# Kernel optimization log

Hardware: AMD Instinct MI355X
Metric: run time of the kernel (lower is better)

The kernel has to match this reference:

```python
import jax, jax.numpy as jnp
import numpy as np

WS = 7    # window_size
SS = 3    # shift_size
NH = 12   # num_heads


def _rel_index(ws):
    # doublestepseq(2*Ww-1, Wh, 1, Ww): seq1[:,None]+seq2[None,:] -> (1, N)
    seq1 = np.arange(ws) * (2 * ws - 1)
    coords = (seq1[:, None] + np.arange(ws)[None, :]).reshape(1, -1)  # (1, N)
    rel = coords + coords.T          # (N, N)
    return np.ascontiguousarray(rel[:, ::-1])  # flip along axis 1


def _attn_mask(Hp, Wp, ws, ss):
    img = np.zeros((Hp, Wp), np.int32)
    cnt = 0
    for h in (slice(0, -ws), slice(-ws, -ss), slice(-ss, None)):
        for w in (slice(0, -ws), slice(-ws, -ss), slice(-ss, None)):
            img[h, w] = cnt
            cnt += 1
    mw = img.reshape(Hp // ws, ws, Wp // ws, ws).transpose(0, 2, 1, 3).reshape(-1, ws * ws)
    diff = mw[:, None, :] - mw[:, :, None]  # unsqueeze(1) - unsqueeze(2)
    return np.where(diff != 0, -100.0, 0.0).astype(np.float32)  # (nW, N, N)


def setup_inputs() -> dict:
    key = jax.random.key(0)
    ks = jax.random.split(key, 4)
    B, H, W, C = 8, 112, 112, 384
    x = jax.random.normal(ks[0], (B, H * W, C), jnp.float32)
    qkv_w = jax.random.normal(ks[1], (C, 3 * C), jnp.float32) * 0.02
    qkv_b = jnp.zeros((3 * C,), jnp.float32)
    proj_w = jax.random.normal(ks[2], (C, C), jnp.float32) * 0.02
    proj_b = jnp.zeros((C,), jnp.float32)
    rel_pos_table = jax.random.normal(ks[3], ((2 * WS - 1) ** 2, NH), jnp.float32) * 0.02
    return {"x": x, "qkv_w": qkv_w, "qkv_b": qkv_b, "proj_w": proj_w,
            "proj_b": proj_b, "rel_pos_table": rel_pos_table, "H": H, "W": W}


def reference(x, qkv_w, qkv_b, proj_w, proj_b, rel_pos_table, H, W):
    B, L, C = x.shape
    hd = C // NH
    scale = hd ** -0.5
    N = WS * WS
    q = x.reshape(B, H, W, C)
    pad_r = (WS - W % WS) % WS
    pad_b = (WS - H % WS) % WS
    q = jnp.pad(q, ((0, 0), (0, pad_b), (0, pad_r), (0, 0)))
    Hp, Wp = H + pad_b, W + pad_r
    # cyclic shift
    sq = jnp.roll(q, (-SS, -SS), axis=(1, 2))
    nWh, nWw = Hp // WS, Wp // WS
    nW = nWh * nWw
    # window partition -> (B*nW, N, C)
    win = sq.reshape(B, nWh, WS, nWw, WS, C).transpose(0, 1, 3, 2, 4, 5).reshape(-1, N, C)
    Bw = win.shape[0]
    qkv = (win @ qkv_w + qkv_b).reshape(Bw, N, 3, NH, hd).transpose(2, 0, 3, 1, 4)
    qh, kh, vh = qkv[0], qkv[1], qkv[2]          # (Bw, NH, N, hd)
    attn = jnp.einsum('whnd,whmd->whnm', qh * scale, kh)  # (Bw, NH, N, N)
    # relative position bias
    ridx = _rel_index(WS)
    bias = rel_pos_table[ridx.reshape(-1)].reshape(N, N, NH).transpose(2, 0, 1)
    attn = attn + bias[None]
    # shifted-window mask
    mask = jnp.asarray(_attn_mask(Hp, Wp, WS, SS))  # (nW, N, N)
    attn = attn.reshape(B, nW, NH, N, N) + mask[None, :, None]
    attn = jax.nn.softmax(attn.reshape(Bw, NH, N, N), axis=-1)
    out = jnp.einsum('whnm,whmd->whnd', attn, vh).transpose(0, 2, 1, 3).reshape(Bw, N, C)
    out = out @ proj_w + proj_b
    # window reverse + reverse shift
    sx = out.reshape(B, nWh, nWw, WS, WS, C).transpose(0, 1, 3, 2, 4, 5).reshape(B, Hp, Wp, C)
    xr = jnp.roll(sx, (SS, SS), axis=(1, 2))[:, :H, :W, :]
    return xr.reshape(B, H * W, C)
```

## Files before the change

kernel.cpp:

```cpp
#include <hip/hip_runtime.h>


typedef __bf16 bf16;
typedef __bf16 bf16x8 __attribute__((ext_vector_type(8)));
typedef float  f32x4  __attribute__((ext_vector_type(4)));

#define MFMA16(a, b, c) __builtin_amdgcn_mfma_f32_16x16x32_bf16((a), (b), (c), 0, 0, 0)

static __device__ __forceinline__ bf16x8 cvt8(const float4 lo, const float4 hi) {
    bf16x8 r;
    r[0] = (bf16)lo.x; r[1] = (bf16)lo.y; r[2] = (bf16)lo.z; r[3] = (bf16)lo.w;
    r[4] = (bf16)hi.x; r[5] = (bf16)hi.y; r[6] = (bf16)hi.z; r[7] = (bf16)hi.w;
    return r;
}

__global__ __launch_bounds__(256) void k0_prep(
    const float* __restrict__ qkv_w, const float* __restrict__ proj_w,
    const float* __restrict__ rpt,
    bf16* __restrict__ w1t, bf16* __restrict__ w2t, float* __restrict__ BT)
{
    unsigned tid = blockIdx.x * 256u + threadIdx.x;
    if (tid < 442368u) {
        unsigned n = tid / 384u, k = tid - n * 384u;
        float v = qkv_w[k * 1152u + n];
        if (n < 384u) v *= 0.17677669529663687f;
        w1t[tid] = (bf16)v;
    } else if (tid < 589824u) {
        unsigned i = tid - 442368u;
        unsigned n = i / 384u, k = i - n * 384u;
        w2t[i] = (bf16)proj_w[k * 384u + n];
    } else if (tid < 638976u) {
        unsigned i = tid - 589824u;
        unsigned h = i >> 12, r = i & 4095u, b = r >> 6, a = r & 63u;
        float v;
        if (b >= 49u) v = -1e9f;
        else if (a >= 49u) v = 0.0f;
        else {
            int ia = (int)(a / 7u), ja = (int)(a - 7u * (a / 7u));
            int ib = (int)(b / 7u), jb = (int)(b - 7u * (b / 7u));
            int ridx = 84 + 13 * (ia - ib) + (ja - jb);
            v = rpt[ridx * 12 + (int)h];
        }
        BT[i] = v;
    }
}

__global__ __launch_bounds__(256) void k0x_cvt(
    const float* __restrict__ X, bf16* __restrict__ Xb)
{
    size_t base = ((size_t)blockIdx.x * 256u + threadIdx.x) * 8u;
    float4 lo = *(const float4*)(X + base);
    float4 hi = *(const float4*)(X + base + 4);
    *(bf16x8*)(Xb + base) = cvt8(lo, hi);
}

__global__ __launch_bounds__(256, 3) void k1_qkv_b(
    const bf16* __restrict__ X, const bf16* __restrict__ W,
    const float* __restrict__ bias, bf16* __restrict__ Y)
{
    __shared__ __align__(16) bf16 Bs[24576];
    unsigned id = blockIdx.x;
    unsigned xcd = id & 7u, seq = id >> 3;
    unsigned mi = seq / 18u, nb = seq - mi * 18u;
    unsigned mblk = xcd + (mi << 3);
    unsigned tid = threadIdx.x;
    unsigned lane = tid & 63u, wv = tid >> 6;
    unsigned ln = lane & 15u, lq = lane >> 4;
    unsigned m0 = mblk * 256u, n0 = nb * 64u;

    for (unsigned c = tid; c < 3072u; c += 256u) {
        unsigned row = c / 48u, kc = c - row * 48u, k = kc * 8u;
        unsigned blk = (k >> 5) * 4u + (row >> 4);
        unsigned l = (row & 15u) | ((kc & 3u) << 4);
        *(int4*)&Bs[(blk * 64u + l) * 8u] = *(const int4*)(W + (size_t)(n0 + row) * 384u + k);
    }
    __syncthreads();

    f32x4 acc[4][4] = {};
    unsigned rbase = m0 + wv * 64u;
    const bf16* Ab = X + (size_t)(rbase + ln) * 384u + lq * 8u;

    bf16x8 af[3][4];
#pragma unroll
    for (unsigned i = 0; i < 4; ++i) af[0][i] = *(const bf16x8*)(Ab + i * 6144u);
#pragma unroll
    for (unsigned i = 0; i < 4; ++i) af[1][i] = *(const bf16x8*)(Ab + 32u + i * 6144u);

#pragma unroll
    for (unsigned kt = 0; kt < 12; ++kt) {
        if (kt < 10u) {
#pragma unroll
            for (unsigned i = 0; i < 4; ++i)
                af[(kt + 2u) % 3u][i] =
                    *(const bf16x8*)(Ab + (kt + 2u) * 32u + i * 6144u);
        }
        bf16x8 bfr[4];
#pragma unroll
        for (unsigned j = 0; j < 4; ++j)
            bfr[j] = *(const bf16x8*)&Bs[((kt * 4u + j) * 64u + lane) * 8u];
#pragma unroll
        for (unsigned i = 0; i < 4; ++i)
#pragma unroll
            for (unsigned j = 0; j < 4; ++j)
                acc[i][j] = MFMA16(af[kt % 3u][i], bfr[j], acc[i][j]);
    }

    float bv[4];
#pragma unroll
    for (unsigned j = 0; j < 4; ++j) {
        unsigned col = n0 + j * 16u + ln;
        bv[j] = bias[col];
        if (col < 384u) bv[j] *= 0.17677669529663687f;
    }

    __syncthreads();
#pragma unroll
    for (unsigned i = 0; i < 4; ++i)
#pragma unroll
        for (unsigned j = 0; j < 4; ++j)
#pragma unroll
            for (unsigned rg = 0; rg < 4; ++rg) {
                unsigned r = wv * 64u + i * 16u + lq * 4u + rg;
                Bs[r * 72u + j * 16u + ln] = (bf16)(acc[i][j][rg] + bv[j]);
            }
    __syncthreads();

#pragma unroll
    for (unsigned it = 0; it < 8; ++it) {
        unsigned idx = it * 256u + tid;
        unsigned row = idx >> 3, c8 = (idx & 7u) * 8u;
        *(bf16x8*)(Y + (size_t)(m0 + row) * 1152u + n0 + c8) =
            *(const bf16x8*)&Bs[row * 72u + c8];
    }
}

__global__ __launch_bounds__(256, 3) void k1_qkv(
    const float* __restrict__ X, const bf16* __restrict__ W,
    const float* __restrict__ bias, bf16* __restrict__ Y)
{
    __shared__ __align__(16) bf16 Bs[24576];
    unsigned id = blockIdx.x;
    unsigned xcd = id & 7u, seq = id >> 3;
    unsigned mi = seq / 18u, nb = seq - mi * 18u;
    unsigned mblk = xcd + (mi << 3);
    unsigned tid = threadIdx.x;
    unsigned lane = tid & 63u, wv = tid >> 6;
    unsigned ln = lane & 15u, lq = lane >> 4;
    unsigned m0 = mblk * 256u, n0 = nb * 64u;

    for (unsigned c = tid; c < 3072u; c += 256u) {
        unsigned row = c / 48u, kc = c - row * 48u, k = kc * 8u;
        unsigned blk = (k >> 5) * 4u + (row >> 4);
        unsigned l = (row & 15u) | ((kc & 3u) << 4);
        *(int4*)&Bs[(blk * 64u + l) * 8u] = *(const int4*)(W + (size_t)(n0 + row) * 384u + k);
    }
    __syncthreads();

    f32x4 acc[4][4] = {};
    unsigned rbase = m0 + wv * 64u;

#pragma unroll
    for (unsigned kt = 0; kt < 12; ++kt) {
        bf16x8 af[4], bfr[4];
#pragma unroll
        for (unsigned i = 0; i < 4; ++i) {
            const float* p = X + (size_t)(rbase + i * 16u + ln) * 384u + kt * 32u + lq * 8u;
            af[i] = cvt8(*(const float4*)p, *(const float4*)(p + 4));
        }
#pragma unroll
        for (unsigned j = 0; j < 4; ++j)
            bfr[j] = *(const bf16x8*)&Bs[((kt * 4u + j) * 64u + lane) * 8u];
#pragma unroll
        for (unsigned i = 0; i < 4; ++i)
#pragma unroll
            for (unsigned j = 0; j < 4; ++j)
                acc[i][j] = MFMA16(af[i], bfr[j], acc[i][j]);
    }

#pragma unroll
    for (unsigned j = 0; j < 4; ++j) {
        unsigned col = n0 + j * 16u + ln;
        float bv = bias[col];
        if (col < 384u) bv *= 0.17677669529663687f;
#pragma unroll
        for (unsigned i = 0; i < 4; ++i) {
            unsigned row = rbase + i * 16u + lq * 4u;
#pragma unroll
            for (unsigned rg = 0; rg < 4; ++rg)
                Y[(size_t)(row + rg) * 1152u + col] = (bf16)(acc[i][j][rg] + bv);
        }
    }
}

__global__ __launch_bounds__(64) void k2_attn(
    bf16* __restrict__ Y, const float* __restrict__ BT)
{
    __shared__ __align__(16) bf16 Pl[64 * 72];
    __shared__ __align__(16) bf16 Vt[32 * 72];
    unsigned h = blockIdx.x, bwin = blockIdx.y;
    unsigned bb = bwin >> 8, wi = bwin & 255u, wh = wi >> 4, ww = wi & 15u;
    unsigned lane = threadIdx.x, ln = lane & 15u, lq = lane >> 4;
    unsigned hw32 = h * 32u;

    auto pixrow = [&](unsigned t) -> unsigned {
        unsigned ti = t / 7u, tj = t - ti * 7u;
        unsigned gh = wh * 7u + ti + 3u; if (gh >= 112u) gh -= 112u;
        unsigned gw = ww * 7u + tj + 3u; if (gw >= 112u) gw -= 112u;
        return bb * 12544u + gh * 112u + gw;
    };

    {
        unsigned t = lane < 49u ? lane : 0u;
        const bf16* vs = Y + (size_t)pixrow(t) * 1152u + 768u + hw32;
        bf16x8 v0 = *(const bf16x8*)(vs);
        bf16x8 v1 = *(const bf16x8*)(vs + 8);
        bf16x8 v2 = *(const bf16x8*)(vs + 16);
        bf16x8 v3 = *(const bf16x8*)(vs + 24);
#pragma unroll
        for (int d = 0; d < 8; ++d) {
            Vt[(unsigned)(d     ) * 72u + lane] = v0[d];
            Vt[(unsigned)(d + 8 ) * 72u + lane] = v1[d];
            Vt[(unsigned)(d + 16) * 72u + lane] = v2[d];
            Vt[(unsigned)(d + 24) * 72u + lane] = v3[d];
        }
    }

    bf16x8 qf[4], kf[4];
#pragma unroll
    for (int i = 0; i < 4; ++i) {
        unsigned t = (unsigned)i * 16u + ln; t = t < 49u ? t : 0u;
        qf[i] = *(const bf16x8*)(Y + (size_t)pixrow(t) * 1152u + hw32 + lq * 8u);
    }
#pragma unroll
    for (int i = 0; i < 4; ++i) {
        unsigned t = (unsigned)i * 16u + ln; t = t < 49u ? t : 0u;
        kf[i] = *(const bf16x8*)(Y + (size_t)pixrow(t) * 1152u + 384u + hw32 + lq * 8u);
    }

    f32x4 s[4][4] = {};
#pragma unroll
    for (int i = 0; i < 4; ++i)
#pragma unroll
        for (int j = 0; j < 4; ++j)
            s[i][j] = MFMA16(qf[i], kf[j], s[i][j]);

    const float* bth = BT + h * 4096u;
#pragma unroll
    for (int i = 0; i < 4; ++i)
#pragma unroll
        for (int j = 0; j < 4; ++j) {
            f32x4 b = *(const f32x4*)(bth + ((unsigned)j * 16u + ln) * 64u +
                                      (unsigned)i * 16u + lq * 4u);
            s[i][j] += b;
        }

    if (wh == 15u || ww == 15u) {
        int ra[4][4], rb[4];
#pragma unroll
        for (int i = 0; i < 4; ++i)
#pragma unroll
            for (int rg = 0; rg < 4; ++rg) {
                unsigned a = (unsigned)i * 16u + lq * 4u + (unsigned)rg;
                unsigned ti = a / 7u, tj = a - ti * 7u;
                unsigned gh = wh * 7u + ti, gw = ww * 7u + tj;
                int rh = gh < 105u ? 0 : (gh < 109u ? 1 : 2);
                int rw = gw < 105u ? 0 : (gw < 109u ? 1 : 2);
                ra[i][rg] = rh * 3 + rw;
            }
#pragma unroll
        for (int j = 0; j < 4; ++j) {
            unsigned bc = (unsigned)j * 16u + ln;
            unsigned ti = bc / 7u, tj = bc - ti * 7u;
            unsigned gh = wh * 7u + ti, gw = ww * 7u + tj;
            int rh = gh < 105u ? 0 : (gh < 109u ? 1 : 2);
            int rw = gw < 105u ? 0 : (gw < 109u ? 1 : 2);
            rb[j] = rh * 3 + rw;
        }
#pragma unroll
        for (int i = 0; i < 4; ++i)
#pragma unroll
            for (int j = 0; j < 4; ++j)
#pragma unroll
                for (int rg = 0; rg < 4; ++rg)
                    if (ra[i][rg] != rb[j]) s[i][j][rg] -= 100.0f;
    }

    float rinv[4][4];
#pragma unroll
    for (int i = 0; i < 4; ++i)
#pragma unroll
        for (int rg = 0; rg < 4; ++rg) {
            float m = fmaxf(fmaxf(s[i][0][rg], s[i][1][rg]),
                            fmaxf(s[i][2][rg], s[i][3][rg]));
#pragma unroll
            for (int d = 8; d >= 1; d >>= 1) m = fmaxf(m, __shfl_xor(m, d, 64));
            float sum = 0.0f;
#pragma unroll
            for (int j = 0; j < 4; ++j) {
                float e = __expf(s[i][j][rg] - m);
                s[i][j][rg] = e;
                sum += e;
            }
#pragma unroll
            for (int d = 8; d >= 1; d >>= 1) sum += __shfl_xor(sum, d, 64);
            rinv[i][rg] = 1.0f / sum;
        }

#pragma unroll
    for (int i = 0; i < 4; ++i)
#pragma unroll
        for (int rg = 0; rg < 4; ++rg) {
            unsigned a = (unsigned)i * 16u + lq * 4u + (unsigned)rg;
#pragma unroll
            for (int j = 0; j < 4; ++j)
                Pl[a * 72u + (unsigned)j * 16u + ln] = (bf16)s[i][j][rg];
        }

    __syncthreads();

    f32x4 o[4][2] = {};
#pragma unroll
    for (int ks = 0; ks < 2; ++ks) {
        bf16x8 pf[4], vf[2];
#pragma unroll
        for (int i = 0; i < 4; ++i)
            pf[i] = *(const bf16x8*)&Pl[((unsigned)i * 16u + ln) * 72u +
                                        (unsigned)ks * 32u + lq * 8u];
#pragma unroll
        for (int c = 0; c < 2; ++c)
            vf[c] = *(const bf16x8*)&Vt[((unsigned)c * 16u + ln) * 72u +
                                        (unsigned)ks * 32u + lq * 8u];
#pragma unroll
        for (int i = 0; i < 4; ++i)
#pragma unroll
            for (int c = 0; c < 2; ++c)
                o[i][c] = MFMA16(pf[i], vf[c], o[i][c]);
    }

#pragma unroll
    for (int i = 0; i < 4; ++i)
#pragma unroll
        for (int rg = 0; rg < 4; ++rg) {
            unsigned a = (unsigned)i * 16u + lq * 4u + (unsigned)rg;
            if (a < 49u) {
                float ri = rinv[i][rg];
                size_t base = (size_t)pixrow(a) * 1152u + hw32;
                Y[base + ln]       = (bf16)(o[i][0][rg] * ri);
                Y[base + 16u + ln] = (bf16)(o[i][1][rg] * ri);
            }
        }
}

__global__ __launch_bounds__(256, 3) void k3_proj(
    const bf16* __restrict__ A, const bf16* __restrict__ W,
    const float* __restrict__ bias, float* __restrict__ Out)
{
    __shared__ __align__(16) bf16 Bs[24576];
    unsigned id = blockIdx.x;
    unsigned xcd = id & 7u, seq = id >> 3;
    unsigned mi = seq / 6u, nb = seq - mi * 6u;
    unsigned mblk = xcd + (mi << 3);
    unsigned tid = threadIdx.x;
    unsigned lane = tid & 63u, wv = tid >> 6;
    unsigned ln = lane & 15u, lq = lane >> 4;
    unsigned m0 = mblk * 256u, n0 = nb * 64u;

    for (unsigned c = tid; c < 3072u; c += 256u) {
        unsigned row = c / 48u, kc = c - row * 48u, k = kc * 8u;
        unsigned blk = (k >> 5) * 4u + (row >> 4);
        unsigned l = (row & 15u) | ((kc & 3u) << 4);
        *(int4*)&Bs[(blk * 64u + l) * 8u] = *(const int4*)(W + (size_t)(n0 + row) * 384u + k);
    }
    __syncthreads();

    f32x4 acc[4][4] = {};
    unsigned rbase = m0 + wv * 64u;

#pragma unroll
    for (unsigned kt = 0; kt < 12; ++kt) {
        bf16x8 af[4], bfr[4];
#pragma unroll
        for (unsigned i = 0; i < 4; ++i)
            af[i] = *(const bf16x8*)(A + (size_t)(rbase + i * 16u + ln) * 1152u +
                                     kt * 32u + lq * 8u);
#pragma unroll
        for (unsigned j = 0; j < 4; ++j)
            bfr[j] = *(const bf16x8*)&Bs[((kt * 4u + j) * 64u + lane) * 8u];
#pragma unroll
        for (unsigned i = 0; i < 4; ++i)
#pragma unroll
            for (unsigned j = 0; j < 4; ++j)
                acc[i][j] = MFMA16(af[i], bfr[j], acc[i][j]);
    }

#pragma unroll
    for (unsigned j = 0; j < 4; ++j) {
        unsigned col = n0 + j * 16u + ln;
        float bv = bias[col];
#pragma unroll
        for (unsigned i = 0; i < 4; ++i) {
            unsigned row = rbase + i * 16u + lq * 4u;
#pragma unroll
            for (unsigned rg = 0; rg < 4; ++rg)
                Out[(size_t)(row + rg) * 384u + col] = acc[i][j][rg] + bv;
        }
    }
}

extern "C" void kernel_launch(void* const* d_in, const int* in_sizes, int n_in,
                              void* d_out, int out_size, void* d_ws, size_t ws_size,
                              hipStream_t stream) {
    const float* x      = (const float*)d_in[0];
    const float* qkv_w  = (const float*)d_in[1];
    const float* qkv_b  = (const float*)d_in[2];
    const float* proj_w = (const float*)d_in[3];
    const float* proj_b = (const float*)d_in[4];
    const float* rpt    = (const float*)d_in[5];
    (void)in_sizes; (void)n_in; (void)out_size;

    char* ws = (char*)d_ws;
    bf16*  Y   = (bf16*)(ws);
    bf16*  w1t = (bf16*)(ws + 231211008u);
    bf16*  w2t = (bf16*)(ws + 232095744u);
    float* BT  = (float*)(ws + 232390656u);
    bf16*  Xb  = (bf16*)(ws + 232587264u);
    float* out = (float*)d_out;

    k0_prep<<<2496, 256, 0, stream>>>(qkv_w, proj_w, rpt, w1t, w2t, BT);
    if (ws_size >= 309657600ull) {
        k0x_cvt<<<18816, 256, 0, stream>>>(x, Xb);
        k1_qkv_b<<<7056, 256, 0, stream>>>(Xb, w1t, qkv_b, Y);
    } else {
        k1_qkv<<<7056, 256, 0, stream>>>(x, w1t, qkv_b, Y);
    }
    k2_attn<<<dim3(12, 2048), 64, 0, stream>>>(Y, BT);
    k3_proj<<<2352, 256, 0, stream>>>(Y, w2t, proj_b, out);
}
```

Baseline: 679.3 us.

## Halve GEMM shared-memory tiles by staging weights in two K halves, raise occupancy

```diff
diff --git a/kernel.cpp b/kernel.cpp
--- a/kernel.cpp
+++ b/kernel.cpp
@@ -54,11 +54,11 @@
     *(bf16x8*)(Xb + base) = cvt8(lo, hi);
 }
 
-__global__ __launch_bounds__(256, 3) void k1_qkv_b(
+__global__ __launch_bounds__(256, 6) void k1_qkv_b(
     const bf16* __restrict__ X, const bf16* __restrict__ W,
     const float* __restrict__ bias, bf16* __restrict__ Y)
 {
-    __shared__ __align__(16) bf16 Bs[24576];
+    __shared__ __align__(16) bf16 Bs[12288];
     unsigned id = blockIdx.x;
     unsigned xcd = id & 7u, seq = id >> 3;
     unsigned mi = seq / 18u, nb = seq - mi * 18u;
@@ -68,13 +68,13 @@
     unsigned ln = lane & 15u, lq = lane >> 4;
     unsigned m0 = mblk * 256u, n0 = nb * 64u;
 
-    for (unsigned c = tid; c < 3072u; c += 256u) {
-        unsigned row = c / 48u, kc = c - row * 48u, k = kc * 8u;
-        unsigned blk = (k >> 5) * 4u + (row >> 4);
+    for (unsigned c = tid; c < 1536u; c += 256u) {
+        unsigned row = c / 24u, kc = c - row * 24u, lk = kc * 8u;
+        unsigned blk = (lk >> 5) * 4u + (row >> 4);
         unsigned l = (row & 15u) | ((kc & 3u) << 4);
-        *(int4*)&Bs[(blk * 64u + l) * 8u] = *(const int4*)(W + (size_t)(n0 + row) * 384u + k);
-    }
-    __syncthreads();
+        *(int4*)&Bs[(blk * 64u + l) * 8u] =
+            *(const int4*)(W + (size_t)(n0 + row) * 384u + lk);
+    }
 
     f32x4 acc[4][4] = {};
     unsigned rbase = m0 + wv * 64u;
@@ -86,18 +86,46 @@
 #pragma unroll
     for (unsigned i = 0; i < 4; ++i) af[1][i] = *(const bf16x8*)(Ab + 32u + i * 6144u);
 
-#pragma unroll
-    for (unsigned kt = 0; kt < 12; ++kt) {
-        if (kt < 10u) {
-#pragma unroll
-            for (unsigned i = 0; i < 4; ++i)
-                af[(kt + 2u) % 3u][i] =
-                    *(const bf16x8*)(Ab + (kt + 2u) * 32u + i * 6144u);
-        }
+    __syncthreads();
+
+#pragma unroll
+    for (unsigned kt = 0; kt < 6; ++kt) {
+#pragma unroll
+        for (unsigned i = 0; i < 4; ++i)
+            af[(kt + 2u) % 3u][i] = *(const bf16x8*)(Ab + (kt + 2u) * 32u + i * 6144u);
         bf16x8 bfr[4];
 #pragma unroll
         for (unsigned j = 0; j < 4; ++j)
             bfr[j] = *(const bf16x8*)&Bs[((kt * 4u + j) * 64u + lane) * 8u];
+#pragma unroll
+        for (unsigned i = 0; i < 4; ++i)
+#pragma unroll
+            for (unsigned j = 0; j < 4; ++j)
+                acc[i][j] = MFMA16(af[kt % 3u][i], bfr[j], acc[i][j]);
+    }
+
+    __syncthreads();
+
+    for (unsigned c = tid; c < 1536u; c += 256u) {
+        unsigned row = c / 24u, kc = c - row * 24u, lk = kc * 8u;
+        unsigned blk = (lk >> 5) * 4u + (row >> 4);
+        unsigned l = (row & 15u) | ((kc & 3u) << 4);
+        *(int4*)&Bs[(blk * 64u + l) * 8u] =
+            *(const int4*)(W + (size_t)(n0 + row) * 384u + 192u + lk);
+    }
+    __syncthreads();
+
+#pragma unroll
+    for (unsigned kt = 6; kt < 12; ++kt) {
+        if (kt < 10u) {
+#pragma unroll
+            for (unsigned i = 0; i < 4; ++i)
+                af[(kt + 2u) % 3u][i] = *(const bf16x8*)(Ab + (kt + 2u) * 32u + i * 6144u);
+        }
+        bf16x8 bfr[4];
+#pragma unroll
+        for (unsigned j = 0; j < 4; ++j)
+            bfr[j] = *(const bf16x8*)&Bs[(((kt - 6u) * 4u + j) * 64u + lane) * 8u];
 #pragma unroll
         for (unsigned i = 0; i < 4; ++i)
 #pragma unroll
@@ -115,80 +143,28 @@
 
     __syncthreads();
 #pragma unroll
-    for (unsigned i = 0; i < 4; ++i)
-#pragma unroll
-        for (unsigned j = 0; j < 4; ++j)
-#pragma unroll
-            for (unsigned rg = 0; rg < 4; ++rg) {
-                unsigned r = wv * 64u + i * 16u + lq * 4u + rg;
-                Bs[r * 72u + j * 16u + ln] = (bf16)(acc[i][j][rg] + bv[j]);
-            }
-    __syncthreads();
-
-#pragma unroll
-    for (unsigned it = 0; it < 8; ++it) {
-        unsigned idx = it * 256u + tid;
-        unsigned row = idx >> 3, c8 = (idx & 7u) * 8u;
-        *(bf16x8*)(Y + (size_t)(m0 + row) * 1152u + n0 + c8) =
-            *(const bf16x8*)&Bs[row * 72u + c8];
-    }
-}
-
-__global__ __launch_bounds__(256, 3) void k1_qkv(
-    const float* __restrict__ X, const bf16* __restrict__ W,
-    const float* __restrict__ bias, bf16* __restrict__ Y)
-{
-    __shared__ __align__(16) bf16 Bs[24576];
-    unsigned id = blockIdx.x;
-    unsigned xcd = id & 7u, seq = id >> 3;
-    unsigned mi = seq / 18u, nb = seq - mi * 18u;
-    unsigned mblk = xcd + (mi << 3);
-    unsigned tid = threadIdx.x;
-    unsigned lane = tid & 63u, wv = tid >> 6;
-    unsigned ln = lane & 15u, lq = lane >> 4;
-    unsigned m0 = mblk * 256u, n0 = nb * 64u;
-
-    for (unsigned c = tid; c < 3072u; c += 256u) {
-        unsigned row = c / 48u, kc = c - row * 48u, k = kc * 8u;
-        unsigned blk = (k >> 5) * 4u + (row >> 4);
-        unsigned l = (row & 15u) | ((kc & 3u) << 4);
-        *(int4*)&Bs[(blk * 64u + l) * 8u] = *(const int4*)(W + (size_t)(n0 + row) * 384u + k);
-    }
-    __syncthreads();
-
-    f32x4 acc[4][4] = {};
-    unsigned rbase = m0 + wv * 64u;
-
-#pragma unroll
-    for (unsigned kt = 0; kt < 12; ++kt) {
-        bf16x8 af[4], bfr[4];
-#pragma unroll
-        for (unsigned i = 0; i < 4; ++i) {
-            const float* p = X + (size_t)(rbase + i * 16u + ln) * 384u + kt * 32u + lq * 8u;
-            af[i] = cvt8(*(const float4*)p, *(const float4*)(p + 4));
-        }
-#pragma unroll
-        for (unsigned j = 0; j < 4; ++j)
-            bfr[j] = *(const bf16x8*)&Bs[((kt * 4u + j) * 64u + lane) * 8u];
-#pragma unroll
-        for (unsigned i = 0; i < 4; ++i)
-#pragma unroll
-            for (unsigned j = 0; j < 4; ++j)
-                acc[i][j] = MFMA16(af[i], bfr[j], acc[i][j]);
-    }
-
-#pragma unroll
-    for (unsigned j = 0; j < 4; ++j) {
-        unsigned col = n0 + j * 16u + ln;
-        float bv = bias[col];
-        if (col < 384u) bv *= 0.17677669529663687f;
-#pragma unroll
-        for (unsigned i = 0; i < 4; ++i) {
-            unsigned row = rbase + i * 16u + lq * 4u;
-#pragma unroll
-            for (unsigned rg = 0; rg < 4; ++rg)
-                Y[(size_t)(row + rg) * 1152u + col] = (bf16)(acc[i][j][rg] + bv);
-        }
+    for (unsigned p = 0; p < 2; ++p) {
+        if ((wv >> 1) == p) {
+            unsigned rloc = (wv & 1u) * 64u;
+#pragma unroll
+            for (unsigned i = 0; i < 4; ++i)
+#pragma unroll
+                for (unsigned j = 0; j < 4; ++j)
+#pragma unroll
+                    for (unsigned rg = 0; rg < 4; ++rg) {
+                        unsigned r = rloc + i * 16u + lq * 4u + rg;
+                        Bs[r * 72u + j * 16u + ln] = (bf16)(acc[i][j][rg] + bv[j]);
+                    }
+        }
+        __syncthreads();
+#pragma unroll
+        for (unsigned it = 0; it < 4; ++it) {
+            unsigned idx = it * 256u + tid;
+            unsigned row = idx >> 3, c8 = (idx & 7u) * 8u;
+            *(bf16x8*)(Y + (size_t)(m0 + p * 128u + row) * 1152u + n0 + c8) =
+                *(const bf16x8*)&Bs[row * 72u + c8];
+        }
+        __syncthreads();
     }
 }
 
@@ -351,11 +327,11 @@
         }
 }
 
-__global__ __launch_bounds__(256, 3) void k3_proj(
+__global__ __launch_bounds__(256, 6) void k3_proj(
     const bf16* __restrict__ A, const bf16* __restrict__ W,
     const float* __restrict__ bias, float* __restrict__ Out)
 {
-    __shared__ __align__(16) bf16 Bs[24576];
+    __shared__ __align__(16) bf16 Bs[12288];
     unsigned id = blockIdx.x;
     unsigned xcd = id & 7u, seq = id >> 3;
     unsigned mi = seq / 6u, nb = seq - mi * 6u;
@@ -365,24 +341,32 @@
     unsigned ln = lane & 15u, lq = lane >> 4;
     unsigned m0 = mblk * 256u, n0 = nb * 64u;
 
-    for (unsigned c = tid; c < 3072u; c += 256u) {
-        unsigned row = c / 48u, kc = c - row * 48u, k = kc * 8u;
-        unsigned blk = (k >> 5) * 4u + (row >> 4);
+    for (unsigned c = tid; c < 1536u; c += 256u) {
+        unsigned row = c / 24u, kc = c - row * 24u, lk = kc * 8u;
+        unsigned blk = (lk >> 5) * 4u + (row >> 4);
         unsigned l = (row & 15u) | ((kc & 3u) << 4);
-        *(int4*)&Bs[(blk * 64u + l) * 8u] = *(const int4*)(W + (size_t)(n0 + row) * 384u + k);
-    }
-    __syncthreads();
+        *(int4*)&Bs[(blk * 64u + l) * 8u] =
+            *(const int4*)(W + (size_t)(n0 + row) * 384u + lk);
+    }
 
     f32x4 acc[4][4] = {};
     unsigned rbase = m0 + wv * 64u;
-
-#pragma unroll
-    for (unsigned kt = 0; kt < 12; ++kt) {
-        bf16x8 af[4], bfr[4];
-#pragma unroll
-        for (unsigned i = 0; i < 4; ++i)
-            af[i] = *(const bf16x8*)(A + (size_t)(rbase + i * 16u + ln) * 1152u +
-                                     kt * 32u + lq * 8u);
+    const bf16* Ab = A + (size_t)(rbase + ln) * 1152u + lq * 8u;
+
+    bf16x8 af[3][4];
+#pragma unroll
+    for (unsigned i = 0; i < 4; ++i) af[0][i] = *(const bf16x8*)(Ab + i * 18432u);
+#pragma unroll
+    for (unsigned i = 0; i < 4; ++i) af[1][i] = *(const bf16x8*)(Ab + 32u + i * 18432u);
+
+    __syncthreads();
+
+#pragma unroll
+    for (unsigned kt = 0; kt < 6; ++kt) {
+#pragma unroll
+        for (unsigned i = 0; i < 4; ++i)
+            af[(kt + 2u) % 3u][i] = *(const bf16x8*)(Ab + (kt + 2u) * 32u + i * 18432u);
+        bf16x8 bfr[4];
 #pragma unroll
         for (unsigned j = 0; j < 4; ++j)
             bfr[j] = *(const bf16x8*)&Bs[((kt * 4u + j) * 64u + lane) * 8u];
@@ -390,7 +374,36 @@
         for (unsigned i = 0; i < 4; ++i)
 #pragma unroll
             for (unsigned j = 0; j < 4; ++j)
-                acc[i][j] = MFMA16(af[i], bfr[j], acc[i][j]);
+                acc[i][j] = MFMA16(af[kt % 3u][i], bfr[j], acc[i][j]);
+    }
+
+    __syncthreads();
+
+    for (unsigned c = tid; c < 1536u; c += 256u) {
+        unsigned row = c / 24u, kc = c - row * 24u, lk = kc * 8u;
+        unsigned blk = (lk >> 5) * 4u + (row >> 4);
+        unsigned l = (row & 15u) | ((kc & 3u) << 4);
+        *(int4*)&Bs[(blk * 64u + l) * 8u] =
+            *(const int4*)(W + (size_t)(n0 + row) * 384u + 192u + lk);
+    }
+    __syncthreads();
+
+#pragma unroll
+    for (unsigned kt = 6; kt < 12; ++kt) {
+        if (kt < 10u) {
+#pragma unroll
+            for (unsigned i = 0; i < 4; ++i)
+                af[(kt + 2u) % 3u][i] = *(const bf16x8*)(Ab + (kt + 2u) * 32u + i * 18432u);
+        }
+        bf16x8 bfr[4];
+#pragma unroll
+        for (unsigned j = 0; j < 4; ++j)
+            bfr[j] = *(const bf16x8*)&Bs[(((kt - 6u) * 4u + j) * 64u + lane) * 8u];
+#pragma unroll
+        for (unsigned i = 0; i < 4; ++i)
+#pragma unroll
+            for (unsigned j = 0; j < 4; ++j)
+                acc[i][j] = MFMA16(af[kt % 3u][i], bfr[j], acc[i][j]);
     }
 
 #pragma unroll
@@ -416,7 +429,7 @@
     const float* proj_w = (const float*)d_in[3];
     const float* proj_b = (const float*)d_in[4];
     const float* rpt    = (const float*)d_in[5];
-    (void)in_sizes; (void)n_in; (void)out_size;
+    (void)in_sizes; (void)n_in; (void)out_size; (void)ws_size;
 
     char* ws = (char*)d_ws;
     bf16*  Y   = (bf16*)(ws);
@@ -427,12 +440,8 @@
     float* out = (float*)d_out;
 
     k0_prep<<<2496, 256, 0, stream>>>(qkv_w, proj_w, rpt, w1t, w2t, BT);
-    if (ws_size >= 309657600ull) {
-        k0x_cvt<<<18816, 256, 0, stream>>>(x, Xb);
-        k1_qkv_b<<<7056, 256, 0, stream>>>(Xb, w1t, qkv_b, Y);
-    } else {
-        k1_qkv<<<7056, 256, 0, stream>>>(x, w1t, qkv_b, Y);
-    }
+    k0x_cvt<<<18816, 256, 0, stream>>>(x, Xb);
+    k1_qkv_b<<<7056, 256, 0, stream>>>(Xb, w1t, qkv_b, Y);
     k2_attn<<<dim3(12, 2048), 64, 0, stream>>>(Y, BT);
     k3_proj<<<2352, 256, 0, stream>>>(Y, w2t, proj_b, out);
 }
```

After: 1.822 ms. 168% more time.
